# Kernel tuning notes

Hardware: AMD Instinct MI355X
Metric: run time of the kernel (lower is better)

## Reference

```python
import jax, jax.numpy as jnp
import numpy as np

B, C, N = 16, 32, 131072


def setup_inputs() -> dict:
    key = jax.random.key(0)
    k1, k2 = jax.random.split(key)
    pred = jax.random.normal(k1, (B, C, N), dtype=jnp.float32)
    true = jax.random.randint(k2, (B, N), 0, C, dtype=jnp.int32)
    return {"pred": pred, "true": true}


def reference(pred, true):
    """FPCELossV3.

    Torch loop semantics: for class i, pos_i are the point indices n (over ALL
    batch rows, with multiplicity) where true[b', n] == i; the term
    -log(p)/p at pred[b, i, n] is summed over every batch b and every such
    occurrence. Equivalent to weighting f(pred[b, i, n]) by
    count[i, n] = sum_{b'} [true[b', n] == i].
    """
    Bc, Cc, Nc = pred.shape
    logp = jax.nn.log_softmax(pred, axis=1)          # (B,C,N)
    p = jnp.exp(logp)
    f = -logp / p                                    # -log(p)/p, (B,C,N)
    # count[c, n] = number of batch rows b' with true[b', n] == c
    counts = jnp.sum(jax.nn.one_hot(true, Cc, dtype=pred.dtype), axis=0).T  # (C,N)
    loss = jnp.sum(f * counts[None, :, :]) / Nc
    return loss
```

## Files before the change

### kernel.cpp

```cpp
#include <hip/hip_runtime.h>


#define B_TOT 16
#define C_CLS 32
#define TPB   256

__global__ __launch_bounds__(TPB) void fpce_kernel(
    const float* __restrict__ pred, const int* __restrict__ tru,
    float* __restrict__ out, int N, float invN) {
  const int n = blockIdx.x * TPB + threadIdx.x;

  int t[B_TOT];
#pragma unroll
  for (int j = 0; j < B_TOT; ++j) t[j] = tru[(size_t)j * N + n];

  float S[B_TOT], T0[B_TOT], T1[B_TOT];
#pragma unroll
  for (int j = 0; j < B_TOT; ++j) { S[j] = 0.f; T0[j] = 0.f; T1[j] = 0.f; }

  const float* p0 = pred + n;

#pragma unroll 4
  for (int c = 0; c < C_CLS; ++c) {
    float x[B_TOT];
#pragma unroll
    for (int j = 0; j < B_TOT; ++j)
      x[j] = p0[(size_t)(j * C_CLS + c) * N];

    int cnt = 0;
#pragma unroll
    for (int j = 0; j < B_TOT; ++j) cnt += (t[j] == c);
    const float cf = (float)cnt;

#pragma unroll
    for (int j = 0; j < B_TOT; ++j) {
      S[j] += __expf(x[j]);
      const float u = cf * __expf(-x[j]);
      T0[j] += u;
      T1[j] = fmaf(u, x[j], T1[j]);
    }
  }

  float W = 0.f;
#pragma unroll
  for (int j = 0; j < B_TOT; ++j) {
    const float L = __logf(S[j]);
    W += S[j] * (L * T0[j] - T1[j]);
  }
  W *= invN;

#pragma unroll
  for (int off = 32; off > 0; off >>= 1) W += __shfl_down(W, off, 64);
  if ((threadIdx.x & 63) == 0) atomicAdd(out, W);
}

extern "C" void kernel_launch(void* const* d_in, const int* in_sizes, int n_in,
                              void* d_out, int out_size, void* d_ws, size_t ws_size,
                              hipStream_t stream) {
  const float* pred = (const float*)d_in[0];
  const int*   tru  = (const int*)d_in[1];
  float*       out  = (float*)d_out;

  const int N = in_sizes[1] / B_TOT;

  hipMemsetAsync(out, 0, sizeof(float), stream);
  fpce_kernel<<<N / TPB, TPB, 0, stream>>>(pred, tru, out, N, 1.0f / (float)N);
}
```

Baseline: 373.7 us.

## Precompute per-class counts and parallelize main kernel over batch with float4 loads

```diff
diff --git a/kernel.cpp b/kernel.cpp
--- a/kernel.cpp
+++ b/kernel.cpp
@@ -4,48 +4,59 @@
 #define B_TOT 16
 #define C_CLS 32
 #define TPB   256
+#define TILE  1024
 
-__global__ __launch_bounds__(TPB) void fpce_kernel(
-    const float* __restrict__ pred, const int* __restrict__ tru,
-    float* __restrict__ out, int N, float invN) {
+__global__ __launch_bounds__(TPB) void fpce_counts(
+    const int* __restrict__ tru, unsigned char* __restrict__ cnt, int N) {
   const int n = blockIdx.x * TPB + threadIdx.x;
-
   int t[B_TOT];
 #pragma unroll
   for (int j = 0; j < B_TOT; ++j) t[j] = tru[(size_t)j * N + n];
+#pragma unroll
+  for (int c = 0; c < C_CLS; ++c) {
+    int k = 0;
+#pragma unroll
+    for (int j = 0; j < B_TOT; ++j) k += (t[j] == c);
+    cnt[(size_t)c * N + n] = (unsigned char)k;
+  }
+}
 
-  float S[B_TOT], T0[B_TOT], T1[B_TOT];
+__global__ __launch_bounds__(TPB, 8) void fpce_main(
+    const float* __restrict__ pred, const unsigned char* __restrict__ cnt,
+    float* __restrict__ out, int N, float invN) {
+  const int b    = blockIdx.x & (B_TOT - 1);
+  const int tile = blockIdx.x >> 4;
+  const int n0   = tile * TILE + threadIdx.x * 4;
+
+  const float*         p = pred + (size_t)b * C_CLS * N + n0;
+  const unsigned char* q = cnt + n0;
+
+  float S[4]  = {0.f, 0.f, 0.f, 0.f};
+  float T0[4] = {0.f, 0.f, 0.f, 0.f};
+  float T1[4] = {0.f, 0.f, 0.f, 0.f};
+
+#pragma unroll 2
+  for (int c = 0; c < C_CLS; ++c) {
+    const float4 x = *(const float4*)(p + (size_t)c * N);
+    const unsigned int w = *(const unsigned int*)(q + (size_t)c * N);
+
+    const float xa[4] = {x.x, x.y, x.z, x.w};
+    const float cf[4] = {(float)(w & 0xffu),        (float)((w >> 8) & 0xffu),
+                         (float)((w >> 16) & 0xffu), (float)(w >> 24)};
 #pragma unroll
-  for (int j = 0; j < B_TOT; ++j) { S[j] = 0.f; T0[j] = 0.f; T1[j] = 0.f; }
-
-  const float* p0 = pred + n;
-
-#pragma unroll 4
-  for (int c = 0; c < C_CLS; ++c) {
-    float x[B_TOT];
-#pragma unroll
-    for (int j = 0; j < B_TOT; ++j)
-      x[j] = p0[(size_t)(j * C_CLS + c) * N];
-
-    int cnt = 0;
-#pragma unroll
-    for (int j = 0; j < B_TOT; ++j) cnt += (t[j] == c);
-    const float cf = (float)cnt;
-
-#pragma unroll
-    for (int j = 0; j < B_TOT; ++j) {
-      S[j] += __expf(x[j]);
-      const float u = cf * __expf(-x[j]);
-      T0[j] += u;
-      T1[j] = fmaf(u, x[j], T1[j]);
+    for (int v = 0; v < 4; ++v) {
+      S[v] += __expf(xa[v]);
+      const float u = cf[v] * __expf(-xa[v]);
+      T0[v] += u;
+      T1[v] = fmaf(u, xa[v], T1[v]);
     }
   }
 
   float W = 0.f;
 #pragma unroll
-  for (int j = 0; j < B_TOT; ++j) {
-    const float L = __logf(S[j]);
-    W += S[j] * (L * T0[j] - T1[j]);
+  for (int v = 0; v < 4; ++v) {
+    const float L = __logf(S[v]);
+    W += S[v] * (L * T0[v] - T1[v]);
   }
   W *= invN;
 
@@ -57,12 +68,15 @@
 extern "C" void kernel_launch(void* const* d_in, const int* in_sizes, int n_in,
                               void* d_out, int out_size, void* d_ws, size_t ws_size,
                               hipStream_t stream) {
-  const float* pred = (const float*)d_in[0];
-  const int*   tru  = (const int*)d_in[1];
-  float*       out  = (float*)d_out;
+  const float*   pred = (const float*)d_in[0];
+  const int*     tru  = (const int*)d_in[1];
+  float*         out  = (float*)d_out;
+  unsigned char* cnt  = (unsigned char*)d_ws;
 
   const int N = in_sizes[1] / B_TOT;
 
   hipMemsetAsync(out, 0, sizeof(float), stream);
-  fpce_kernel<<<N / TPB, TPB, 0, stream>>>(pred, tru, out, N, 1.0f / (float)N);
+  fpce_counts<<<N / TPB, TPB, 0, stream>>>(tru, cnt, N);
+  fpce_main<<<B_TOT * (N / TILE), TPB, 0, stream>>>(pred, cnt, out, N,
+                                                    1.0f / (float)N);
 }
```

Result: slower. 432.8 us (+15.8%).
